# Kernel tuning notes

Hardware: AMD Instinct MI355X
Metric: run time of the kernel (lower is better)

## Reference

```python
import jax, jax.numpy as jnp
import numpy as np

RADIUS = 2  # module init kwarg


def _lga(cost, weights, r):
    """One local-guided-aggregation pass.
    cost:    [B, D, H, W]
    weights: [B, 3*K*K, H, W], K = 2r+1; group 0/1/2 weight disparity d-1/d/d+1.
    """
    B, D, H, W = cost.shape
    K = 2 * r + 1
    # zero-pad: disparity by 1 (for d-1 / d+1), spatial by r (window)
    cp = jnp.pad(cost, ((0, 0), (1, 1), (r, r), (r, r)))
    w = weights.reshape(B, 3, K * K, H, W)
    out = jnp.zeros_like(cost)
    for idx in range(K * K):
        i, j = idx // K, idx % K
        # window view: cp[:, :, y+i, x+j] == cost[:, :, y+i-r, x+j-r]
        win = cp[:, :, i:i + H, j:j + W]          # [B, D+2, H, W]
        out = out + (w[:, 0, idx][:, None] * win[:, 0:D]        # cost[d-1]
                     + w[:, 1, idx][:, None] * win[:, 1:D + 1]  # cost[d]
                     + w[:, 2, idx][:, None] * win[:, 2:D + 2]) # cost[d+1]
    return out


def setup_inputs() -> dict:
    key = jax.random.key(0)
    k1, k2 = jax.random.split(key)
    B, D, H, W = 2, 64, 384, 768
    K = 2 * RADIUS + 1
    input1 = jax.random.normal(k1, (B, D, H, W), dtype=jnp.float32)
    # aggregation stays numerically tame (mimics normalized guidance)
    input2 = jax.random.uniform(k2, (B, 3 * K * K, H, W), dtype=jnp.float32) * (1.0 / (3 * K * K))
    return {"input1": input1, "input2": input2}


def reference(input1, input2):
    out = input1
    for _ in range(3):  # LGA3 = three sequential LGA passes, same weights
        out = _lga(out, input2, RADIUS)
    return out
```

## Files before the change

### kernel.cpp

```cpp
#include <hip/hip_runtime.h>


#define B_ 2
#define D_ 64
#define H_ 384
#define W_ 768
static constexpr int HW    = H_ * W_;
static constexpr int DPT   = 8;
static constexpr int NTY   = 4;
static constexpr int WT    = 64;
static constexpr int HSEG  = 8;
static constexpr int RITER = HSEG + 4;
static constexpr int LROW  = 72;
static constexpr int LRWS  = 34;
static constexpr int NGRAN = LRWS * 18;
static constexpr int NCH   = 10;
static constexpr int LBUF  = NCH * 256;

__device__ __forceinline__ void gld_lds16(const float* g, float* l) {
  __builtin_amdgcn_global_load_lds((const __attribute__((address_space(1))) unsigned int*)g,
                                   (__attribute__((address_space(3))) unsigned int*)l,
                                   16, 0, 0);
}

__global__ __launch_bounds__(256, 1) void lga_pass(const float* __restrict__ src,
                                                   const float* __restrict__ wts,
                                                   float* __restrict__ dst) {
  __shared__ float cl[2][LBUF];

  const int tx    = threadIdx.x;
  const int ty    = threadIdx.y;
  const int bx    = blockIdx.x;
  const int w0    = bx * WT, w = w0 + tx;
  const int hs    = blockIdx.y * HSEG;
  const int b     = blockIdx.z >> 1;
  const int dhalf = blockIdx.z & 1;
  const int dbase = dhalf * 32 - 1;
  const int d0    = dhalf * 32 + ty * DPT;

  const float* sb  = src + (size_t)b * D_ * HW;
  const float* wtb = wts + (size_t)b * 75 * HW;

  const bool has_lo = (d0 > 0);
  const bool has_hi = (d0 + DPT < D_);
  const bool edge   = (bx == 0) || (bx == W_ / WT - 1);

  auto stage = [&](int buf, int h_in) {
#pragma unroll
    for (int q = 0; q < 3; ++q) {
      const int c = ty + q * 4;
      if (c < NCH) {
        int G = c * 64 + tx;
        G = G > NGRAN - 1 ? NGRAN - 1 : G;
        const int p  = G / 18;
        const int k  = G - p * 18;
        int pd = dbase + p;
        pd = pd < 0 ? 0 : (pd > D_ - 1 ? D_ - 1 : pd);
        long idx = (long)pd * HW + (long)h_in * W_ + (w0 - 4) + (k << 2);
        idx = idx < 0 ? 0 : idx;
        const long mx = (long)D_ * HW - 4;
        idx = idx > mx ? mx : idx;
        gld_lds16(sb + idx, &cl[buf][c * 256]);
      }
    }
  };

  {
    const int h0 = hs - 2;
    if (h0 >= 0) stage(0, h0);
  }
  __syncthreads();

  float acc[5][DPT];
#pragma unroll
  for (int s = 0; s < 5; ++s)
#pragma unroll
    for (int k = 0; k < DPT; ++k) acc[s][k] = 0.f;

  int n = 0;
#pragma unroll 1
  for (int r = 0; r < RITER; ++r) {
    float W[75];
#pragma unroll
    for (int s = 0; s < 5; ++s) {
      if ((unsigned)(r - 4 + s) < (unsigned)HSEG) {
        const int o     = hs + r - 4 + s;
        const int ib    = (4 - s) * 5;
        const float* wr = wtb + (size_t)o * W_;
#pragma unroll
        for (int g = 0; g < 3; ++g)
#pragma unroll
          for (int j = 0; j < 5; ++j)
            W[s * 15 + g * 5 + j] = wr[(size_t)(ib + j + 25 * g) * HW + w];
      }
    }

    if (r + 1 < RITER) {
      const int h_nx = hs - 2 + r + 1;
      if ((unsigned)h_nx < (unsigned)H_) stage(n ^ 1, h_nx);
    }

    const int  h_in = hs - 2 + r;
    const bool hv   = (unsigned)h_in < (unsigned)H_;
    float vv[5][DPT + 2];
    if (hv) {
      const float* vbase = cl[n] + ty * DPT * LROW + tx + 2;
      if (!edge) {
#pragma unroll
        for (int j = 0; j < 5; ++j)
#pragma unroll
          for (int m = 0; m < DPT + 2; ++m)
            vv[j][m] = vbase[m * LROW + j];
        if (!has_lo) {
#pragma unroll
          for (int j = 0; j < 5; ++j) vv[j][0] = 0.f;
        }
        if (!has_hi) {
#pragma unroll
          for (int j = 0; j < 5; ++j) vv[j][DPT + 1] = 0.f;
        }
      } else {
#pragma unroll
        for (int j = 0; j < 5; ++j) {
          const bool wokj = (unsigned)(w + j - 2) < (unsigned)W_;
#pragma unroll
          for (int m = 0; m < DPT + 2; ++m) {
            const float v = vbase[m * LROW + j];
            bool ok = wokj;
            if (m == 0)       ok = ok && has_lo;
            if (m == DPT + 1) ok = ok && has_hi;
            vv[j][m] = ok ? v : 0.f;
          }
        }
      }
    }

#pragma unroll
    for (int s = 0; s < 5; ++s) {
      if (hv && (unsigned)(r - 4 + s) < (unsigned)HSEG) {
#pragma unroll
        for (int j = 0; j < 5; ++j)
#pragma unroll
          for (int k = 0; k < DPT; ++k)
            acc[s][k] = fmaf(W[s * 15 + j],      vv[j][k],
                        fmaf(W[s * 15 + 5 + j],  vv[j][k + 1],
                        fmaf(W[s * 15 + 10 + j], vv[j][k + 2], acc[s][k])));
      }
    }

    if (r >= 4) {
      const int o = hs + r - 4;
#pragma unroll
      for (int k = 0; k < DPT; ++k) {
        float* dp = dst + (((size_t)b * D_ + d0 + k) * H_ + o) * W_;
        dp[w] = acc[0][k];
      }
    }

#pragma unroll
    for (int s = 0; s < 4; ++s)
#pragma unroll
      for (int k = 0; k < DPT; ++k) acc[s][k] = acc[s + 1][k];
#pragma unroll
    for (int k = 0; k < DPT; ++k) acc[4][k] = 0.f;

    __syncthreads();
    n ^= 1;
  }
}

extern "C" void kernel_launch(void* const* d_in, const int* in_sizes, int n_in,
                              void* d_out, int out_size, void* d_ws, size_t ws_size,
                              hipStream_t stream) {
  const float* cost = (const float*)d_in[0];
  const float* wts  = (const float*)d_in[1];
  float* out = (float*)d_out;
  float* ws  = (float*)d_ws;

  dim3 grid(W_ / WT, H_ / HSEG, B_ * 2);
  dim3 block(WT, NTY);

  lga_pass<<<grid, block, 0, stream>>>(cost, wts, out);
  lga_pass<<<grid, block, 0, stream>>>(out, wts, ws);
  lga_pass<<<grid, block, 0, stream>>>(ws, wts, out);
}
```

Measured before the change: 552.8 us.

## Stage guidance weights through LDS and drop cost-row double buffering

Weights are no longer loaded per-thread into 75 registers. They are now staged into shared memory with async global-to-LDS loads, one shared tile that all four d-groups in the block read, which cuts redundant global weight reads and register pressure. The cost-row staging loses its double buffer and becomes a single buffer loaded in the same iteration, followed by a barrier. This exposes load latency on every row, since the prefetch overlap with compute is gone.

```diff
diff --git a/kernel.cpp b/kernel.cpp
--- a/kernel.cpp
+++ b/kernel.cpp
@@ -14,8 +14,9 @@
 static constexpr int LROW  = 72;
 static constexpr int LRWS  = 34;
 static constexpr int NGRAN = LRWS * 18;
-static constexpr int NCH   = 10;
-static constexpr int LBUF  = NCH * 256;
+static constexpr int NCH_C = 10;
+static constexpr int NCH_W = 19;
+static constexpr int WCH   = 76;
 
 __device__ __forceinline__ void gld_lds16(const float* g, float* l) {
   __builtin_amdgcn_global_load_lds((const __attribute__((address_space(1))) unsigned int*)g,
@@ -26,7 +27,8 @@
 __global__ __launch_bounds__(256, 1) void lga_pass(const float* __restrict__ src,
                                                    const float* __restrict__ wts,
                                                    float* __restrict__ dst) {
-  __shared__ float cl[2][LBUF];
+  __shared__ float cl[NCH_C * 256];
+  __shared__ float wl[WCH * 64];
 
   const int tx    = threadIdx.x;
   const int ty    = threadIdx.y;
@@ -45,66 +47,62 @@
   const bool has_hi = (d0 + DPT < D_);
   const bool edge   = (bx == 0) || (bx == W_ / WT - 1);
 
-  auto stage = [&](int buf, int h_in) {
-#pragma unroll
-    for (int q = 0; q < 3; ++q) {
-      const int c = ty + q * 4;
-      if (c < NCH) {
-        int G = c * 64 + tx;
-        G = G > NGRAN - 1 ? NGRAN - 1 : G;
-        const int p  = G / 18;
-        const int k  = G - p * 18;
-        int pd = dbase + p;
-        pd = pd < 0 ? 0 : (pd > D_ - 1 ? D_ - 1 : pd);
-        long idx = (long)pd * HW + (long)h_in * W_ + (w0 - 4) + (k << 2);
-        idx = idx < 0 ? 0 : idx;
-        const long mx = (long)D_ * HW - 4;
-        idx = idx > mx ? mx : idx;
-        gld_lds16(sb + idx, &cl[buf][c * 256]);
-      }
-    }
-  };
-
-  {
-    const int h0 = hs - 2;
-    if (h0 >= 0) stage(0, h0);
-  }
-  __syncthreads();
-
   float acc[5][DPT];
 #pragma unroll
   for (int s = 0; s < 5; ++s)
 #pragma unroll
     for (int k = 0; k < DPT; ++k) acc[s][k] = 0.f;
 
-  int n = 0;
 #pragma unroll 1
   for (int r = 0; r < RITER; ++r) {
-    float W[75];
+    {
+      int h_in = hs - 2 + r;
+      h_in = h_in < 0 ? 0 : (h_in >= H_ ? H_ - 1 : h_in);
 #pragma unroll
-    for (int s = 0; s < 5; ++s) {
-      if ((unsigned)(r - 4 + s) < (unsigned)HSEG) {
-        const int o     = hs + r - 4 + s;
-        const int ib    = (4 - s) * 5;
-        const float* wr = wtb + (size_t)o * W_;
+      for (int q = 0; q < 3; ++q) {
+        const int c = ty + q * 4;
+        if (c < NCH_C) {
+          int G = c * 64 + tx;
+          G = G > NGRAN - 1 ? NGRAN - 1 : G;
+          const int p = G / 18;
+          const int k = G - p * 18;
+          int pd = dbase + p;
+          pd = pd < 0 ? 0 : (pd > D_ - 1 ? D_ - 1 : pd);
+          long idx = (long)pd * HW + (long)h_in * W_ + (w0 - 4) + (k << 2);
+          idx = idx < 0 ? 0 : idx;
+          const long mx = (long)D_ * HW - 4;
+          idx = idx > mx ? mx : idx;
+          gld_lds16(sb + idx, &cl[c * 256]);
+        }
+      }
+    }
+    {
 #pragma unroll
-        for (int g = 0; g < 3; ++g)
-#pragma unroll
-          for (int j = 0; j < 5; ++j)
-            W[s * 15 + g * 5 + j] = wr[(size_t)(ib + j + 25 * g) * HW + w];
+      for (int q = 0; q < 5; ++q) {
+        const int ci = ty + q * 4;
+        if (ci < NCH_W) {
+          int ch = ci * 4 + (tx >> 4);
+          ch = ch > 74 ? 74 : ch;
+          const int s  = ch / 15;
+          const int t  = ch - s * 15;
+          const int g  = t / 5;
+          const int j  = t - g * 5;
+          const int cw = (4 - s) * 5 + j + g * 25;
+          int o = hs + r - 4 + s;
+          o = o < 0 ? 0 : (o >= H_ ? H_ - 1 : o);
+          const float* p = wtb + (size_t)cw * HW + (size_t)o * W_ + w0 + ((tx & 15) << 2);
+          gld_lds16(p, &wl[ci * 256]);
+        }
       }
     }
 
-    if (r + 1 < RITER) {
-      const int h_nx = hs - 2 + r + 1;
-      if ((unsigned)h_nx < (unsigned)H_) stage(n ^ 1, h_nx);
-    }
+    __syncthreads();
 
     const int  h_in = hs - 2 + r;
     const bool hv   = (unsigned)h_in < (unsigned)H_;
     float vv[5][DPT + 2];
     if (hv) {
-      const float* vbase = cl[n] + ty * DPT * LROW + tx + 2;
+      const float* vbase = cl + ty * DPT * LROW + tx + 2;
       if (!edge) {
 #pragma unroll
         for (int j = 0; j < 5; ++j)
@@ -138,13 +136,18 @@
 #pragma unroll
     for (int s = 0; s < 5; ++s) {
       if (hv && (unsigned)(r - 4 + s) < (unsigned)HSEG) {
+        const float* wsl = wl + s * 15 * 64 + tx;
 #pragma unroll
-        for (int j = 0; j < 5; ++j)
+        for (int j = 0; j < 5; ++j) {
+          const float w0v = wsl[(j)      * 64];
+          const float w1v = wsl[(5 + j)  * 64];
+          const float w2v = wsl[(10 + j) * 64];
 #pragma unroll
           for (int k = 0; k < DPT; ++k)
-            acc[s][k] = fmaf(W[s * 15 + j],      vv[j][k],
-                        fmaf(W[s * 15 + 5 + j],  vv[j][k + 1],
-                        fmaf(W[s * 15 + 10 + j], vv[j][k + 2], acc[s][k])));
+            acc[s][k] = fmaf(w0v, vv[j][k],
+                        fmaf(w1v, vv[j][k + 1],
+                        fmaf(w2v, vv[j][k + 2], acc[s][k])));
+        }
       }
     }
 
@@ -165,7 +168,6 @@
     for (int k = 0; k < DPT; ++k) acc[4][k] = 0.f;
 
     __syncthreads();
-    n ^= 1;
   }
 }
 
```

Measured after the change: 552.4 us. No clear change (-0.1%).

## Give each wavefront private LDS staging and replace block barriers with vmcnt waits

Applied to the files above, without the earlier changes.

The shared LDS staging of the block's disparity planes is split into per-wavefront private buffers. Each wave now stages its own 10 disparity planes (d0-1..d0+8) for the next row via global_load_lds. Block-wide __syncthreads are replaced by explicit s_waitcnt vmcnt waits, so waves no longer stall on each other, and the weight loads are moved after the LDS reads. In exchange, halo planes shared between adjacent waves are loaded twice. Correctness also now depends on hand-written vmcnt counts matching the exact order in which loads and stores are issued.

```diff
diff --git a/kernel.cpp b/kernel.cpp
--- a/kernel.cpp
+++ b/kernel.cpp
@@ -11,11 +11,11 @@
 static constexpr int WT    = 64;
 static constexpr int HSEG  = 8;
 static constexpr int RITER = HSEG + 4;
-static constexpr int LROW  = 72;
-static constexpr int LRWS  = 34;
-static constexpr int NGRAN = LRWS * 18;
-static constexpr int NCH   = 10;
-static constexpr int LBUF  = NCH * 256;
+static constexpr int PLW   = 72;
+static constexpr int NPL   = 10;
+static constexpr int NGR   = NPL * 18;
+static constexpr int BUFG  = 192;
+static constexpr int BUFF  = BUFG * 4;
 
 __device__ __forceinline__ void gld_lds16(const float* g, float* l) {
   __builtin_amdgcn_global_load_lds((const __attribute__((address_space(1))) unsigned int*)g,
@@ -26,7 +26,7 @@
 __global__ __launch_bounds__(256, 1) void lga_pass(const float* __restrict__ src,
                                                    const float* __restrict__ wts,
                                                    float* __restrict__ dst) {
-  __shared__ float cl[2][LBUF];
+  __shared__ float cl[NTY][2][BUFF];
 
   const int tx    = threadIdx.x;
   const int ty    = threadIdx.y;
@@ -35,7 +35,6 @@
   const int hs    = blockIdx.y * HSEG;
   const int b     = blockIdx.z >> 1;
   const int dhalf = blockIdx.z & 1;
-  const int dbase = dhalf * 32 - 1;
   const int d0    = dhalf * 32 + ty * DPT;
 
   const float* sb  = src + (size_t)b * D_ * HW;
@@ -45,31 +44,26 @@
   const bool has_hi = (d0 + DPT < D_);
   const bool edge   = (bx == 0) || (bx == W_ / WT - 1);
 
-  auto stage = [&](int buf, int h_in) {
+  auto stage = [&](int bufSel, int h_in) {
 #pragma unroll
     for (int q = 0; q < 3; ++q) {
-      const int c = ty + q * 4;
-      if (c < NCH) {
-        int G = c * 64 + tx;
-        G = G > NGRAN - 1 ? NGRAN - 1 : G;
-        const int p  = G / 18;
-        const int k  = G - p * 18;
-        int pd = dbase + p;
-        pd = pd < 0 ? 0 : (pd > D_ - 1 ? D_ - 1 : pd);
-        long idx = (long)pd * HW + (long)h_in * W_ + (w0 - 4) + (k << 2);
-        idx = idx < 0 ? 0 : idx;
-        const long mx = (long)D_ * HW - 4;
-        idx = idx > mx ? mx : idx;
-        gld_lds16(sb + idx, &cl[buf][c * 256]);
-      }
+      int g = q * 64 + tx;
+      g = g > NGR - 1 ? NGR - 1 : g;
+      const int p = g / 18;
+      const int k = g - p * 18;
+      int pd = d0 - 1 + p;
+      pd = pd < 0 ? 0 : (pd > D_ - 1 ? D_ - 1 : pd);
+      long idx = (long)pd * HW + (long)h_in * W_ + (w0 - 4) + (k << 2);
+      idx = idx < 0 ? 0 : idx;
+      const long mx = (long)D_ * HW - 4;
+      idx = idx > mx ? mx : idx;
+      gld_lds16(sb + idx, &cl[ty][bufSel][q * 256]);
     }
   };
+  auto clampH = [](int h) { return h < 0 ? 0 : (h >= H_ ? H_ - 1 : h); };
 
-  {
-    const int h0 = hs - 2;
-    if (h0 >= 0) stage(0, h0);
-  }
-  __syncthreads();
+  stage(0, clampH(hs - 2));
+  asm volatile("s_waitcnt vmcnt(0)" ::: "memory");
 
   float acc[5][DPT];
 #pragma unroll
@@ -77,40 +71,22 @@
 #pragma unroll
     for (int k = 0; k < DPT; ++k) acc[s][k] = 0.f;
 
-  int n = 0;
 #pragma unroll 1
   for (int r = 0; r < RITER; ++r) {
-    float W[75];
-#pragma unroll
-    for (int s = 0; s < 5; ++s) {
-      if ((unsigned)(r - 4 + s) < (unsigned)HSEG) {
-        const int o     = hs + r - 4 + s;
-        const int ib    = (4 - s) * 5;
-        const float* wr = wtb + (size_t)o * W_;
-#pragma unroll
-        for (int g = 0; g < 3; ++g)
-#pragma unroll
-          for (int j = 0; j < 5; ++j)
-            W[s * 15 + g * 5 + j] = wr[(size_t)(ib + j + 25 * g) * HW + w];
-      }
-    }
-
-    if (r + 1 < RITER) {
-      const int h_nx = hs - 2 + r + 1;
-      if ((unsigned)h_nx < (unsigned)H_) stage(n ^ 1, h_nx);
-    }
+    if (r + 1 < RITER) stage((r + 1) & 1, clampH(hs - 2 + r + 1));
+    asm volatile("" ::: "memory");
 
     const int  h_in = hs - 2 + r;
     const bool hv   = (unsigned)h_in < (unsigned)H_;
     float vv[5][DPT + 2];
     if (hv) {
-      const float* vbase = cl[n] + ty * DPT * LROW + tx + 2;
+      const float* vb = &cl[ty][r & 1][0] + tx + 2;
       if (!edge) {
 #pragma unroll
         for (int j = 0; j < 5; ++j)
 #pragma unroll
           for (int m = 0; m < DPT + 2; ++m)
-            vv[j][m] = vbase[m * LROW + j];
+            vv[j][m] = vb[m * PLW + j];
         if (!has_lo) {
 #pragma unroll
           for (int j = 0; j < 5; ++j) vv[j][0] = 0.f;
@@ -125,13 +101,28 @@
           const bool wokj = (unsigned)(w + j - 2) < (unsigned)W_;
 #pragma unroll
           for (int m = 0; m < DPT + 2; ++m) {
-            const float v = vbase[m * LROW + j];
+            const float v = vb[m * PLW + j];
             bool ok = wokj;
             if (m == 0)       ok = ok && has_lo;
             if (m == DPT + 1) ok = ok && has_hi;
             vv[j][m] = ok ? v : 0.f;
           }
         }
+      }
+    }
+
+    float W[75];
+#pragma unroll
+    for (int s = 0; s < 5; ++s) {
+      if ((unsigned)(r - 4 + s) < (unsigned)HSEG) {
+        const int o     = hs + r - 4 + s;
+        const int ib    = (4 - s) * 5;
+        const float* wr = wtb + (size_t)o * W_;
+#pragma unroll
+        for (int g = 0; g < 3; ++g)
+#pragma unroll
+          for (int j = 0; j < 5; ++j)
+            W[s * 15 + g * 5 + j] = wr[(size_t)(ib + j + 25 * g) * HW + w];
       }
     }
 
@@ -164,8 +155,10 @@
 #pragma unroll
     for (int k = 0; k < DPT; ++k) acc[4][k] = 0.f;
 
-    __syncthreads();
-    n ^= 1;
+    if (r < RITER - 1) {
+      if (r >= 4) { asm volatile("s_waitcnt vmcnt(8)" ::: "memory"); }
+      else        { asm volatile("s_waitcnt vmcnt(0)" ::: "memory"); }
+    }
   }
 }
 
```

Measured after the change: 711.5 us. 1.29x slower.

## Split weight loads per window column to cut register pressure and raise occupancy

Applied to the files above, without the earlier changes.

Restructures the inner loop so the 75 weights and 5x10 cost values per row are no longer held at once. It walks the five window columns in a non-unrolled loop, loading 15 weights and 10 LDS values per column, and drops the launch_bounds min-blocks hint. The aim is to cut VGPR use so more waves fit per CU. The edge/non-edge fast path is merged into a single masked path. The risk is less memory-level parallelism for the weight loads, which are now issued in smaller serialized batches, plus per-column loop overhead.

```diff
diff --git a/kernel.cpp b/kernel.cpp
--- a/kernel.cpp
+++ b/kernel.cpp
@@ -23,9 +23,9 @@
                                    16, 0, 0);
 }
 
-__global__ __launch_bounds__(256, 1) void lga_pass(const float* __restrict__ src,
-                                                   const float* __restrict__ wts,
-                                                   float* __restrict__ dst) {
+__global__ __launch_bounds__(256) void lga_pass(const float* __restrict__ src,
+                                                const float* __restrict__ wts,
+                                                float* __restrict__ dst) {
   __shared__ float cl[2][LBUF];
 
   const int tx    = threadIdx.x;
@@ -43,7 +43,6 @@
 
   const bool has_lo = (d0 > 0);
   const bool has_hi = (d0 + DPT < D_);
-  const bool edge   = (bx == 0) || (bx == W_ / WT - 1);
 
   auto stage = [&](int buf, int h_in) {
 #pragma unroll
@@ -80,21 +79,6 @@
   int n = 0;
 #pragma unroll 1
   for (int r = 0; r < RITER; ++r) {
-    float W[75];
-#pragma unroll
-    for (int s = 0; s < 5; ++s) {
-      if ((unsigned)(r - 4 + s) < (unsigned)HSEG) {
-        const int o     = hs + r - 4 + s;
-        const int ib    = (4 - s) * 5;
-        const float* wr = wtb + (size_t)o * W_;
-#pragma unroll
-        for (int g = 0; g < 3; ++g)
-#pragma unroll
-          for (int j = 0; j < 5; ++j)
-            W[s * 15 + g * 5 + j] = wr[(size_t)(ib + j + 25 * g) * HW + w];
-      }
-    }
-
     if (r + 1 < RITER) {
       const int h_nx = hs - 2 + r + 1;
       if ((unsigned)h_nx < (unsigned)H_) stage(n ^ 1, h_nx);
@@ -102,49 +86,45 @@
 
     const int  h_in = hs - 2 + r;
     const bool hv   = (unsigned)h_in < (unsigned)H_;
-    float vv[5][DPT + 2];
-    if (hv) {
-      const float* vbase = cl[n] + ty * DPT * LROW + tx + 2;
-      if (!edge) {
+    const float* vb = cl[n] + ty * DPT * LROW + tx + 2;
+
+#pragma unroll 1
+    for (int j = 0; j < 5; ++j) {
+      float W[15];
 #pragma unroll
-        for (int j = 0; j < 5; ++j)
-#pragma unroll
-          for (int m = 0; m < DPT + 2; ++m)
-            vv[j][m] = vbase[m * LROW + j];
-        if (!has_lo) {
-#pragma unroll
-          for (int j = 0; j < 5; ++j) vv[j][0] = 0.f;
-        }
-        if (!has_hi) {
-#pragma unroll
-          for (int j = 0; j < 5; ++j) vv[j][DPT + 1] = 0.f;
-        }
-      } else {
-#pragma unroll
-        for (int j = 0; j < 5; ++j) {
-          const bool wokj = (unsigned)(w + j - 2) < (unsigned)W_;
-#pragma unroll
-          for (int m = 0; m < DPT + 2; ++m) {
-            const float v = vbase[m * LROW + j];
-            bool ok = wokj;
-            if (m == 0)       ok = ok && has_lo;
-            if (m == DPT + 1) ok = ok && has_hi;
-            vv[j][m] = ok ? v : 0.f;
-          }
+      for (int s = 0; s < 5; ++s) {
+        if ((unsigned)(r - 4 + s) < (unsigned)HSEG) {
+          const int o  = hs + r - 4 + s;
+          const int ch = (4 - s) * 5 + j;
+          const float* wr = wtb + (size_t)o * W_ + w;
+          W[s * 3 + 0] = wr[(size_t)ch * HW];
+          W[s * 3 + 1] = wr[(size_t)(ch + 25) * HW];
+          W[s * 3 + 2] = wr[(size_t)(ch + 50) * HW];
         }
       }
-    }
+
+      float vv[DPT + 2];
+      if (hv) {
+        const bool wokj = (unsigned)(w + j - 2) < (unsigned)W_;
+#pragma unroll
+        for (int m = 0; m < DPT + 2; ++m) {
+          const float v = vb[m * LROW + j];
+          bool ok = wokj;
+          if (m == 0)       ok = ok && has_lo;
+          if (m == DPT + 1) ok = ok && has_hi;
+          vv[m] = ok ? v : 0.f;
+        }
+      }
 
 #pragma unroll
-    for (int s = 0; s < 5; ++s) {
-      if (hv && (unsigned)(r - 4 + s) < (unsigned)HSEG) {
-#pragma unroll
-        for (int j = 0; j < 5; ++j)
+      for (int s = 0; s < 5; ++s) {
+        if (hv && (unsigned)(r - 4 + s) < (unsigned)HSEG) {
 #pragma unroll
           for (int k = 0; k < DPT; ++k)
-            acc[s][k] = fmaf(W[s * 15 + j],      vv[j][k],
-                        fmaf(W[s * 15 + 5 + j],  vv[j][k + 1],
-                        fmaf(W[s * 15 + 10 + j], vv[j][k + 2], acc[s][k])));
+            acc[s][k] = fmaf(W[s * 3 + 0], vv[k],
+                        fmaf(W[s * 3 + 1], vv[k + 1],
+                        fmaf(W[s * 3 + 2], vv[k + 2], acc[s][k])));
+        }
       }
     }
 
```

Result: slower. 1.019 ms (+84.4%).
